# Performance work log

Hardware: AMD Instinct MI355X
Metric: run time of the kernel (lower is better)

The kernel has to match this reference:

```python
import jax, jax.numpy as jnp
import numpy as np

DIM = 192
HEADS = 6
WS = 8          # window_size
SHIFT = 4       # shift_size = window_size // 2
HID = DIM * 4   # mlp hidden
EPS = 1e-5


def _rel_index(ws):
    coords = np.stack(np.meshgrid(np.arange(ws), np.arange(ws), indexing='ij')).reshape(2, -1)
    rel = coords[:, :, None] - coords[:, None, :]
    rel = rel.transpose(1, 2, 0).copy()
    rel[:, :, 0] += ws - 1
    rel[:, :, 1] += ws - 1
    rel[:, :, 0] *= 2 * ws - 1
    return rel.sum(-1)  # [N, N] int


def _attn_mask(H, W, ws, ss):
    img = np.zeros((H, W), np.float32)
    sl = (slice(0, -ws), slice(-ws, -ss), slice(-ss, None))
    cnt = 0
    for h in sl:
        for w in sl:
            img[h, w] = cnt
            cnt += 1
    mw = img.reshape(H // ws, ws, W // ws, ws).transpose(0, 2, 1, 3).reshape(-1, ws * ws)
    am = mw[:, None, :] - mw[:, :, None]
    return np.where(am != 0, np.float32(-100.0), np.float32(0.0))  # [nW, N, N]


def _ln(x, w, b):
    m = x.mean(-1, keepdims=True)
    v = ((x - m) ** 2).mean(-1, keepdims=True)
    return (x - m) / jnp.sqrt(v + EPS) * w + b


def setup_inputs() -> dict:
    key = jax.random.key(0)
    ks = jax.random.split(key, 8)
    B, H, W = 8, 128, 128
    d = {
        'x': jax.random.normal(ks[0], (B, H * W, DIM), jnp.float32),
        'norm1_w': jnp.ones((DIM,), jnp.float32),
        'norm1_b': jnp.zeros((DIM,), jnp.float32),
        'qkv_w': jax.random.normal(ks[1], (DIM, 3 * DIM), jnp.float32) * 0.02,
        'qkv_b': jnp.zeros((3 * DIM,), jnp.float32),
        'rel_bias': jax.random.normal(ks[2], ((2 * WS - 1) ** 2, HEADS), jnp.float32) * 0.02,
        'proj_w': jax.random.normal(ks[3], (DIM, DIM), jnp.float32) * 0.02,
        'proj_b': jnp.zeros((DIM,), jnp.float32),
        'norm2_w': jnp.ones((DIM,), jnp.float32),
        'norm2_b': jnp.zeros((DIM,), jnp.float32),
        'mlp_w1': jax.random.normal(ks[4], (DIM, HID), jnp.float32) * 0.02,
        'mlp_b1': jnp.zeros((HID,), jnp.float32),
        'mlp_w2': jax.random.normal(ks[5], (HID, DIM), jnp.float32) * 0.02,
        'mlp_b2': jnp.zeros((DIM,), jnp.float32),
        'H': H,
        'W': W,
    }
    return d


def reference(x, norm1_w, norm1_b, qkv_w, qkv_b, rel_bias, proj_w, proj_b,
              norm2_w, norm2_b, mlp_w1, mlp_b1, mlp_w2, mlp_b2, H, W):
    B = x.shape[0]
    C, ws = DIM, WS
    N = ws * ws
    hd = C // HEADS
    shortcut = x
    h = _ln(x, norm1_w, norm1_b).reshape(B, H, W, C)
    if SHIFT > 0:
        h = jnp.roll(h, (-SHIFT, -SHIFT), axis=(1, 2))
    # window partition: (B,H,W,C) -> (B*nW, N, C)
    wins = h.reshape(B, H // ws, ws, W // ws, ws, C).transpose(0, 1, 3, 2, 4, 5).reshape(-1, N, C)
    qkv = (wins @ qkv_w + qkv_b).reshape(-1, N, 3, HEADS, hd).transpose(2, 0, 3, 1, 4)
    q, k, v = qkv[0] * (hd ** -0.5), qkv[1], qkv[2]
    attn = jnp.einsum('bhnd,bhmd->bhnm', q, k)
    ridx = jnp.asarray(_rel_index(ws))
    bias = rel_bias[ridx.reshape(-1)].reshape(N, N, HEADS).transpose(2, 0, 1)
    attn = attn + bias[None]
    if SHIFT > 0:
        am = jnp.asarray(_attn_mask(H, W, ws, SHIFT))  # [nW, N, N]
        nW = am.shape[0]
        attn = (attn.reshape(B, nW, HEADS, N, N) + am[None, :, None]).reshape(-1, HEADS, N, N)
    attn = jax.nn.softmax(attn, axis=-1)
    o = jnp.einsum('bhnm,bhmd->bhnd', attn, v).transpose(0, 2, 1, 3).reshape(-1, N, C)
    o = o @ proj_w + proj_b
    # window reverse: (B*nW, N, C) -> (B, H, W, C)
    o = o.reshape(B, H // ws, W // ws, ws, ws, C).transpose(0, 1, 3, 2, 4, 5).reshape(B, H, W, C)
    if SHIFT > 0:
        o = jnp.roll(o, (SHIFT, SHIFT), axis=(1, 2))
    x = shortcut + o.reshape(B, H * W, C)
    y = _ln(x, norm2_w, norm2_b)
    y = jax.nn.gelu(y @ mlp_w1 + mlp_b1, approximate=False) @ mlp_w2 + mlp_b2
    return x + y
```

## Files before the change

### kernel.cpp

```cpp
#include <hip/hip_runtime.h>
#include <hip/hip_bf16.h>
#include <math.h>

typedef __bf16 bf16;
typedef __bf16 bf16x8 __attribute__((ext_vector_type(8)));
typedef float f32x4 __attribute__((ext_vector_type(4)));

#define EPS 1e-5f

__device__ __forceinline__ int swz16(int row, int byteoff) {
  return byteoff ^ ((row & 7) << 4);
}

__device__ __forceinline__ void st_lds_bf16x2(char* lds, int off, float a, float b) {
  union { bf16 h[2]; unsigned u; } pk;
  pk.h[0] = (bf16)a; pk.h[1] = (bf16)b;
  *(unsigned*)(lds + off) = pk.u;
}

__device__ __forceinline__ void gl_lds16(const bf16* g, char* l) {
  __builtin_amdgcn_global_load_lds(
      (const __attribute__((address_space(1))) unsigned int*)(const void*)g,
      (__attribute__((address_space(3))) unsigned int*)l, 16, 0, 0);
}

__device__ __forceinline__ void bar_raw() {
  asm volatile("" ::: "memory");
  __builtin_amdgcn_s_barrier();
  asm volatile("" ::: "memory");
}

__global__ __launch_bounds__(256) void k_prep(
    const float* __restrict__ qkv_w, const float* __restrict__ proj_w,
    const float* __restrict__ mlp_w1, const float* __restrict__ mlp_w2,
    const float* __restrict__ rel_bias,
    bf16* __restrict__ w_qkv_t, bf16* __restrict__ w_proj_t,
    bf16* __restrict__ w_mlp1_t, bf16* __restrict__ w_mlp2_t,
    float* __restrict__ bias_tab) {
  int idx = blockIdx.x * 256 + threadIdx.x;
  if (idx < 110592) { int n = idx / 192, k = idx % 192; w_qkv_t[idx] = (bf16)qkv_w[k * 576 + n]; return; }
  idx -= 110592;
  if (idx < 36864) { int n = idx / 192, k = idx % 192; w_proj_t[idx] = (bf16)proj_w[k * 192 + n]; return; }
  idx -= 36864;
  if (idx < 147456) { int n = idx / 192, k = idx % 192; w_mlp1_t[idx] = (bf16)mlp_w1[k * 768 + n]; return; }
  idx -= 147456;
  if (idx < 147456) { int n = idx / 768, k = idx % 768; w_mlp2_t[idx] = (bf16)mlp_w2[k * 192 + n]; return; }
  idx -= 147456;
  {
    int h = idx >> 12, n = (idx >> 6) & 63, m = idx & 63;
    int i1 = n >> 3, j1 = n & 7, i2 = m >> 3, j2 = m & 7;
    int ridx = (i1 - i2 + 7) * 15 + (j1 - j2 + 7);
    bias_tab[idx] = rel_bias[ridx * 6 + h];
  }
}

__global__ __launch_bounds__(512) void k1a_ln(
    const float* __restrict__ x, const float* __restrict__ n1w, const float* __restrict__ n1b,
    bf16* __restrict__ xn) {
  const int win = blockIdx.x;
  const int bb = win >> 8, wi = (win >> 4) & 15, wj = win & 15;
  const int tid = threadIdx.x;
  const int t = tid >> 3, q = tid & 7;
  const int i = t >> 3, j = t & 7;
  const int oh = (wi * 8 + i + 4) & 127, ow = (wj * 8 + j + 4) & 127;
  const float* xr = x + (((size_t)bb * 128 + oh) * 128 + ow) * 192 + q * 24;
  float v[24];
  float s = 0.f, ss = 0.f;
#pragma unroll
  for (int u = 0; u < 6; ++u) {
    float4 f = ((const float4*)xr)[u];
    v[4 * u] = f.x; v[4 * u + 1] = f.y; v[4 * u + 2] = f.z; v[4 * u + 3] = f.w;
    s += (f.x + f.y) + (f.z + f.w);
    ss += (f.x * f.x + f.y * f.y) + (f.z * f.z + f.w * f.w);
  }
  s += __shfl_xor(s, 1); s += __shfl_xor(s, 2); s += __shfl_xor(s, 4);
  ss += __shfl_xor(ss, 1); ss += __shfl_xor(ss, 2); ss += __shfl_xor(ss, 4);
  const float mean = s * (1.f / 192.f);
  const float rstd = rsqrtf(ss * (1.f / 192.f) - mean * mean + EPS);
  union { bf16 h[24]; uint4 u4[3]; } pk;
#pragma unroll
  for (int u = 0; u < 24; ++u) {
    const int c = q * 24 + u;
    pk.h[u] = (bf16)((v[u] - mean) * rstd * n1w[c] + n1b[c]);
  }
  uint4* dst = (uint4*)(xn + ((size_t)win * 64 + t) * 192 + q * 24);
#pragma unroll
  for (int u = 0; u < 3; ++u) dst[u] = pk.u4[u];
}

__global__ __launch_bounds__(512, 4) void k1b_qkv(
    const bf16* __restrict__ xn, const bf16* __restrict__ wqkv, const float* __restrict__ qkvb,
    bf16* __restrict__ qbuf, bf16* __restrict__ kbuf, bf16* __restrict__ vtbuf) {
  __shared__ alignas(16) char ldsA[2][16384];
  __shared__ alignas(16) char ldsB[2][24576];
  const int blk = blockIdx.x, cb = blockIdx.y;
  const int tid = threadIdx.x;
  const int wid = tid >> 6, lane = tid & 63, lr = lane & 15, lg = lane >> 4;
  const int wr = wid >> 1, wc = wid & 1;
  const bf16* hA = xn + (size_t)blk * 128 * 192;
  const bf16* wB = wqkv + (size_t)cb * 192 * 192;

  auto stage = [&](int buf, int kt) {
    const int ko = kt * 64;
#pragma unroll
    for (int i = 0; i < 2; ++i) {
      const int slot = i * 512 + wid * 64 + lane;
      const int r = slot >> 3, c = slot & 7;
      gl_lds16(hA + (size_t)r * 192 + ko + ((c ^ (r & 7)) << 3),
               ldsA[buf] + (i * 512 + wid * 64) * 16);
    }
#pragma unroll
    for (int i = 0; i < 3; ++i) {
      const int slot = i * 512 + wid * 64 + lane;
      const int r = slot >> 3, c = slot & 7;
      gl_lds16(wB + (size_t)r * 192 + ko + ((c ^ (r & 7)) << 3),
               ldsB[buf] + (i * 512 + wid * 64) * 16);
    }
  };

  f32x4 acc[2][6] = {};
  stage(0, 0);
  int cur = 0;
  for (int kt = 0; kt < 3; ++kt) {
    if (kt < 2) {
      stage(cur ^ 1, kt + 1);
      asm volatile("s_waitcnt vmcnt(5)" ::: "memory");
    } else {
      asm volatile("s_waitcnt vmcnt(0)" ::: "memory");
    }
    bar_raw();
#pragma unroll
    for (int ks = 0; ks < 2; ++ks) {
      bf16x8 af[2];
#pragma unroll
      for (int rf = 0; rf < 2; ++rf) {
        const int row = wr * 32 + rf * 16 + lr;
        af[rf] = *(const bf16x8*)(ldsA[cur] + row * 128 + (((ks * 4 + lg) ^ (row & 7)) << 4));
      }
#pragma unroll
      for (int cf = 0; cf < 6; ++cf) {
        const int col = wc * 96 + cf * 16 + lr;
        const bf16x8 bfr = *(const bf16x8*)(ldsB[cur] + col * 128 + (((ks * 4 + lg) ^ (col & 7)) << 4));
#pragma unroll
        for (int rf = 0; rf < 2; ++rf)
          acc[rf][cf] = __builtin_amdgcn_mfma_f32_16x16x32_bf16(af[rf], bfr, acc[rf][cf], 0, 0, 0);
      }
    }
    bar_raw();
    cur ^= 1;
  }
  const float scale = 0.1767766952966369f;
  if (cb < 2) {
    bf16* dst = (cb == 0) ? qbuf : kbuf;
    const float sc = (cb == 0) ? scale : 1.f;
#pragma unroll
    for (int rf = 0; rf < 2; ++rf) {
#pragma unroll
      for (int jj = 0; jj < 4; ++jj) {
        const size_t grow = (size_t)blk * 128 + wr * 32 + rf * 16 + lg * 4 + jj;
#pragma unroll
        for (int cf = 0; cf < 6; ++cf) {
          const int col = wc * 96 + cf * 16 + lr;
          dst[grow * 192 + col] = (bf16)((acc[rf][cf][jj] + qkvb[cb * 192 + col]) * sc);
        }
      }
    }
  } else {
    char* vlds = (char*)ldsB;
#pragma unroll
    for (int cf = 0; cf < 6; ++cf) {
      const int col = wc * 96 + cf * 16 + lr;
      const float bias = qkvb[384 + col];
#pragma unroll
      for (int rf = 0; rf < 2; ++rf)
#pragma unroll
        for (int jj = 0; jj < 4; ++jj) {
          const int row = wr * 32 + rf * 16 + lg * 4 + jj;
          *(bf16*)(vlds + swz16(row, row * 384 + col * 2)) = (bf16)(acc[rf][cf][jj] + bias);
        }
    }
    __syncthreads();
#pragma unroll
    for (int it = 0; it < 12; ++it) {
      const int idx = it * 512 + tid;
      const int w = idx / 3072, rem = idx % 3072;
      const int d = rem >> 4, tg = rem & 15;
      union { ushort u[4]; uint2 v; } pk;
#pragma unroll
      for (int j = 0; j < 4; ++j) {
        const int row = w * 64 + tg * 4 + j;
        pk.u[j] = *(const ushort*)(vlds + swz16(row, row * 384 + d * 2));
      }
      const int head = d >> 5, dd = d & 31;
      const int win = blk * 2 + w;
      *(uint2*)(vtbuf + ((size_t)win * 6 + head) * 2048 + dd * 64 + tg * 4) = pk.v;
    }
  }
}

__global__ __launch_bounds__(384) void k2_attn(
    const bf16* __restrict__ qbuf, const bf16* __restrict__ kbuf,
    const bf16* __restrict__ vtbuf, const float* __restrict__ btab_all,
    bf16* __restrict__ obuf) {
  __shared__ alignas(16) char p_lds_all[6 * 64 * 128];
  const int win = blockIdx.x;
  const int head = threadIdx.x >> 6;
  char* p_lds = p_lds_all + head * 64 * 128;
  const int lane = threadIdx.x & 63, lr = lane & 15, lg = lane >> 4;
  const bf16* qb = qbuf + (size_t)win * 12288 + head * 32;
  const bf16* kb = kbuf + (size_t)win * 12288 + head * 32;
  const bf16* vb = vtbuf + ((size_t)win * 6 + head) * 2048;
  f32x4 sacc[4][4] = {};
  bf16x8 bk[4];
#pragma unroll
  for (int cf = 0; cf < 4; ++cf)
    bk[cf] = *(const bf16x8*)(kb + (size_t)(cf * 16 + lr) * 192 + lg * 8);
#pragma unroll
  for (int rf = 0; rf < 4; ++rf) {
    const bf16x8 aq = *(const bf16x8*)(qb + (size_t)(rf * 16 + lr) * 192 + lg * 8);
#pragma unroll
    for (int cf = 0; cf < 4; ++cf)
      sacc[rf][cf] = __builtin_amdgcn_mfma_f32_16x16x32_bf16(aq, bk[cf], sacc[rf][cf], 0, 0, 0);
  }
  const int wi = (win >> 4) & 15, wj = win & 15;
  const bool eh = (wi == 15), ew = (wj == 15);
  const float* btab = btab_all + head * 4096;
#pragma unroll
  for (int rf = 0; rf < 4; ++rf) {
#pragma unroll
    for (int jj = 0; jj < 4; ++jj) {
      const int n = rf * 16 + lg * 4 + jj;
      const int i1 = n >> 3, j1 = n & 7;
      float vals[4];
#pragma unroll
      for (int cf = 0; cf < 4; ++cf) {
        const int m = cf * 16 + lr;
        const int i2 = m >> 3, j2 = m & 7;
        float sv = sacc[rf][cf][jj] + btab[n * 64 + m];
        const bool msk = (eh && ((i1 >= 4) != (i2 >= 4))) || (ew && ((j1 >= 4) != (j2 >= 4)));
        if (msk) sv -= 100.f;
        vals[cf] = sv;
      }
      float mx = fmaxf(fmaxf(vals[0], vals[1]), fmaxf(vals[2], vals[3]));
      mx = fmaxf(mx, __shfl_xor(mx, 1));
      mx = fmaxf(mx, __shfl_xor(mx, 2));
      mx = fmaxf(mx, __shfl_xor(mx, 4));
      mx = fmaxf(mx, __shfl_xor(mx, 8));
      float sum = 0.f;
#pragma unroll
      for (int cf = 0; cf < 4; ++cf) { vals[cf] = __expf(vals[cf] - mx); sum += vals[cf]; }
      sum += __shfl_xor(sum, 1); sum += __shfl_xor(sum, 2);
      sum += __shfl_xor(sum, 4); sum += __shfl_xor(sum, 8);
      const float inv = 1.f / sum;
#pragma unroll
      for (int cf = 0; cf < 4; ++cf) {
        const int m = cf * 16 + lr;
        *(bf16*)(p_lds + swz16(n, n * 128 + m * 2)) = (bf16)(vals[cf] * inv);
      }
    }
  }
  __syncthreads();
  f32x4 oacc[4][2] = {};
#pragma unroll
  for (int ks = 0; ks < 2; ++ks) {
    bf16x8 pf[4];
#pragma unroll
    for (int rf = 0; rf < 4; ++rf) {
      const int row = rf * 16 + lr;
      pf[rf] = *(const bf16x8*)(p_lds + swz16(row, row * 128 + (ks * 32 + lg * 8) * 2));
    }
#pragma unroll
    for (int cf = 0; cf < 2; ++cf) {
      const bf16x8 vf = *(const bf16x8*)(vb + (cf * 16 + lr) * 64 + ks * 32 + lg * 8);
#pragma unroll
      for (int rf = 0; rf < 4; ++rf)
        oacc[rf][cf] = __builtin_amdgcn_mfma_f32_16x16x32_bf16(pf[rf], vf, oacc[rf][cf], 0, 0, 0);
    }
  }
  bf16* ob = obuf + (size_t)win * 64 * 192 + head * 32;
#pragma unroll
  for (int rf = 0; rf < 4; ++rf)
#pragma unroll
    for (int cf = 0; cf < 2; ++cf)
#pragma unroll
      for (int jj = 0; jj < 4; ++jj) {
        const int tok = rf * 16 + lg * 4 + jj;
        const int d = cf * 16 + lr;
        ob[(size_t)tok * 192 + d] = (bf16)oacc[rf][cf][jj];
      }
}

__global__ __launch_bounds__(512, 4) void k3_proj(
    const bf16* __restrict__ obuf, const bf16* __restrict__ wproj,
    const float* __restrict__ projb, const float* __restrict__ x,
    bf16* __restrict__ x2) {
  __shared__ alignas(16) char ldsA[2][16384];
  __shared__ alignas(16) char ldsB[2][24576];
  const int blk = blockIdx.x;
  const int tid = threadIdx.x;
  const int wid = tid >> 6, lane = tid & 63, lr = lane & 15, lg = lane >> 4;
  const int wr = wid >> 1, wc = wid & 1;
  const bf16* hA = obuf + (size_t)blk * 128 * 192;

  auto stage = [&](int buf, int kt) {
    const int ko = kt * 64;
#pragma unroll
    for (int i = 0; i < 2; ++i) {
      const int slot = i * 512 + wid * 64 + lane;
      const int r = slot >> 3, c = slot & 7;
      gl_lds16(hA + (size_t)r * 192 + ko + ((c ^ (r & 7)) << 3),
               ldsA[buf] + (i * 512 + wid * 64) * 16);
    }
#pragma unroll
    for (int i = 0; i < 3; ++i) {
      const int slot = i * 512 + wid * 64 + lane;
      const int r = slot >> 3, c = slot & 7;
      gl_lds16(wproj + (size_t)r * 192 + ko + ((c ^ (r & 7)) << 3),
               ldsB[buf] + (i * 512 + wid * 64) * 16);
    }
  };

  f32x4 acc[2][6] = {};
  stage(0, 0);
  int cur = 0;
  for (int kt = 0; kt < 3; ++kt) {
    if (kt < 2) {
      stage(cur ^ 1, kt + 1);
      asm volatile("s_waitcnt vmcnt(5)" ::: "memory");
    } else {
      asm volatile("s_waitcnt vmcnt(0)" ::: "memory");
    }
    bar_raw();
#pragma unroll
    for (int ks = 0; ks < 2; ++ks) {
      bf16x8 af[2];
#pragma unroll
      for (int rf = 0; rf < 2; ++rf) {
        const int row = wr * 32 + rf * 16 + lr;
        af[rf] = *(const bf16x8*)(ldsA[cur] + row * 128 + (((ks * 4 + lg) ^ (row & 7)) << 4));
      }
#pragma unroll
      for (int cf = 0; cf < 6; ++cf) {
        const int col = wc * 96 + cf * 16 + lr;
        const bf16x8 bfr = *(const bf16x8*)(ldsB[cur] + col * 128 + (((ks * 4 + lg) ^ (col & 7)) << 4));
#pragma unroll
        for (int rf = 0; rf < 2; ++rf)
          acc[rf][cf] = __builtin_amdgcn_mfma_f32_16x16x32_bf16(af[rf], bfr, acc[rf][cf], 0, 0, 0);
      }
    }
    bar_raw();
    cur ^= 1;
  }
#pragma unroll
  for (int rf = 0; rf < 2; ++rf) {
#pragma unroll
    for (int jj = 0; jj < 4; ++jj) {
      const int grow = blk * 128 + wr * 32 + rf * 16 + lg * 4 + jj;
      const int win = grow >> 6, t = grow & 63;
      const int bb = win >> 8, wi = (win >> 4) & 15, wj = win & 15;
      const int oh = (wi * 8 + (t >> 3) + 4) & 127, ow = (wj * 8 + (t & 7) + 4) & 127;
      const size_t orow = (((size_t)bb * 128 + oh) * 128 + ow) * 192;
#pragma unroll
      for (int cf = 0; cf < 6; ++cf) {
        const int col = wc * 96 + cf * 16 + lr;
        x2[orow + col] = (bf16)(x[orow + col] + acc[rf][cf][jj] + projb[col]);
      }
    }
  }
}

__global__ __launch_bounds__(512) void k4ln(
    const bf16* __restrict__ x2, const float* __restrict__ n2w, const float* __restrict__ n2b,
    bf16* __restrict__ xln) {
  const int tid = threadIdx.x;
  const int t = tid >> 3, q = tid & 7;
  const size_t row = (size_t)blockIdx.x * 64 + t;
  const bf16* xr = x2 + row * 192 + q * 24;
  float v[24];
  float s = 0.f, ss = 0.f;
#pragma unroll
  for (int u = 0; u < 3; ++u) {
    const bf16x8 f = ((const bf16x8*)xr)[u];
#pragma unroll
    for (int e = 0; e < 8; ++e) {
      const float fv = (float)f[e];
      v[8 * u + e] = fv;
      s += fv; ss += fv * fv;
    }
  }
  s += __shfl_xor(s, 1); s += __shfl_xor(s, 2); s += __shfl_xor(s, 4);
  ss += __shfl_xor(ss, 1); ss += __shfl_xor(ss, 2); ss += __shfl_xor(ss, 4);
  const float mean = s * (1.f / 192.f);
  const float rstd = rsqrtf(ss * (1.f / 192.f) - mean * mean + EPS);
  union { bf16 h[24]; uint4 u4[3]; } pk;
#pragma unroll
  for (int u = 0; u < 24; ++u) {
    const int c = q * 24 + u;
    pk.h[u] = (bf16)((v[u] - mean) * rstd * n2w[c] + n2b[c]);
  }
  uint4* dst = (uint4*)(xln + row * 192 + q * 24);
#pragma unroll
  for (int u = 0; u < 3; ++u) dst[u] = pk.u4[u];
}

__global__ __launch_bounds__(512, 4) void k4a_gemm(
    const bf16* __restrict__ xln, const bf16* __restrict__ w1t, const float* __restrict__ b1,
    bf16* __restrict__ h1) {
  __shared__ alignas(16) char ldsA[2][16384];
  __shared__ alignas(16) char ldsB[2][24576];
  const int blk = blockIdx.x, cb = blockIdx.y;
  const int tid = threadIdx.x;
  const int wid = tid >> 6, lane = tid & 63, lr = lane & 15, lg = lane >> 4;
  const int wr = wid >> 1, wc = wid & 1;
  const bf16* hA = xln + (size_t)blk * 128 * 192;
  const bf16* wB = w1t + (size_t)cb * 192 * 192;

  auto stage = [&](int buf, int kt) {
    const int ko = kt * 64;
#pragma unroll
    for (int i = 0; i < 2; ++i) {
      const int slot = i * 512 + wid * 64 + lane;
      const int r = slot >> 3, c = slot & 7;
      gl_lds16(hA + (size_t)r * 192 + ko + ((c ^ (r & 7)) << 3),
               ldsA[buf] + (i * 512 + wid * 64) * 16);
    }
#pragma unroll
    for (int i = 0; i < 3; ++i) {
      const int slot = i * 512 + wid * 64 + lane;
      const int r = slot >> 3, c = slot & 7;
      gl_lds16(wB + (size_t)r * 192 + ko + ((c ^ (r & 7)) << 3),
               ldsB[buf] + (i * 512 + wid * 64) * 16);
    }
  };

  f32x4 acc[2][6] = {};
  stage(0, 0);
  int cur = 0;
  for (int kt = 0; kt < 3; ++kt) {
    if (kt < 2) {
      stage(cur ^ 1, kt + 1);
      asm volatile("s_waitcnt vmcnt(5)" ::: "memory");
    } else {
      asm volatile("s_waitcnt vmcnt(0)" ::: "memory");
    }
    bar_raw();
#pragma unroll
    for (int ks = 0; ks < 2; ++ks) {
      bf16x8 af[2];
#pragma unroll
      for (int rf = 0; rf < 2; ++rf) {
        const int row = wr * 32 + rf * 16 + lr;
        af[rf] = *(const bf16x8*)(ldsA[cur] + row * 128 + (((ks * 4 + lg) ^ (row & 7)) << 4));
      }
#pragma unroll
      for (int cf = 0; cf < 6; ++cf) {
        const int col = wc * 96 + cf * 16 + lr;
        const bf16x8 bfr = *(const bf16x8*)(ldsB[cur] + col * 128 + (((ks * 4 + lg) ^ (col & 7)) << 4));
#pragma unroll
        for (int rf = 0; rf < 2; ++rf)
          acc[rf][cf] = __builtin_amdgcn_mfma_f32_16x16x32_bf16(af[rf], bfr, acc[rf][cf], 0, 0, 0);
      }
    }
    bar_raw();
    cur ^= 1;
  }
#pragma unroll
  for (int rf = 0; rf < 2; ++rf) {
#pragma unroll
    for (int jj = 0; jj < 4; ++jj) {
      const size_t grow = (size_t)blk * 128 + wr * 32 + rf * 16 + lg * 4 + jj;
#pragma unroll
      for (int cf = 0; cf < 6; ++cf) {
        const int col = wc * 96 + cf * 16 + lr;
        const float vv = acc[rf][cf][jj] + b1[cb * 192 + col];
        const float g = 0.5f * vv * (1.f + erff(vv * 0.70710678f));
        h1[grow * 768 + cb * 192 + col] = (bf16)g;
      }
    }
  }
}

__global__ __launch_bounds__(512, 4) void k4b_mlp2(
    const bf16* __restrict__ h1, const bf16* __restrict__ w2t,
    const float* __restrict__ b2, const bf16* __restrict__ x2,
    float* __restrict__ out) {
  __shared__ alignas(16) char ldsA[2][16384];
  __shared__ alignas(16) char ldsB[2][24576];
  const int blk = blockIdx.x;
  const int tid = threadIdx.x;
  const int wid = tid >> 6, lane = tid & 63, lr = lane & 15, lg = lane >> 4;
  const int wr = wid >> 1, wc = wid & 1;
  const bf16* hA = h1 + (size_t)blk * 128 * 768;

  auto stage = [&](int buf, int kt) {
    const int ko = kt * 64;
#pragma unroll
    for (int i = 0; i < 2; ++i) {
      const int slot = i * 512 + wid * 64 + lane;
      const int r = slot >> 3, c = slot & 7;
      gl_lds16(hA + (size_t)r * 768 + ko + ((c ^ (r & 7)) << 3),
               ldsA[buf] + (i * 512 + wid * 64) * 16);
    }
#pragma unroll
    for (int i = 0; i < 3; ++i) {
      const int slot = i * 512 + wid * 64 + lane;
      const int r = slot >> 3, c = slot & 7;
      gl_lds16(w2t + (size_t)r * 768 + ko + ((c ^ (r & 7)) << 3),
               ldsB[buf] + (i * 512 + wid * 64) * 16);
    }
  };

  f32x4 acc[2][6] = {};
  stage(0, 0);
  int cur = 0;
  for (int kt = 0; kt < 12; ++kt) {
    if (kt < 11) {
      stage(cur ^ 1, kt + 1);
      asm volatile("s_waitcnt vmcnt(5)" ::: "memory");
    } else {
      asm volatile("s_waitcnt vmcnt(0)" ::: "memory");
    }
    bar_raw();
#pragma unroll
    for (int ks = 0; ks < 2; ++ks) {
      bf16x8 af[2];
#pragma unroll
      for (int rf = 0; rf < 2; ++rf) {
        const int row = wr * 32 + rf * 16 + lr;
        af[rf] = *(const bf16x8*)(ldsA[cur] + row * 128 + (((ks * 4 + lg) ^ (row & 7)) << 4));
      }
#pragma unroll
      for (int cf = 0; cf < 6; ++cf) {
        const int col = wc * 96 + cf * 16 + lr;
        const bf16x8 bfr = *(const bf16x8*)(ldsB[cur] + col * 128 + (((ks * 4 + lg) ^ (col & 7)) << 4));
#pragma unroll
        for (int rf = 0; rf < 2; ++rf)
          acc[rf][cf] = __builtin_amdgcn_mfma_f32_16x16x32_bf16(af[rf], bfr, acc[rf][cf], 0, 0, 0);
      }
    }
    bar_raw();
    cur ^= 1;
  }
#pragma unroll
  for (int rf = 0; rf < 2; ++rf) {
#pragma unroll
    for (int jj = 0; jj < 4; ++jj) {
      const size_t grow = (size_t)blk * 128 + wr * 32 + rf * 16 + lg * 4 + jj;
#pragma unroll
      for (int cf = 0; cf < 6; ++cf) {
        const int col = wc * 96 + cf * 16 + lr;
        out[grow * 192 + col] = (float)x2[grow * 192 + col] + acc[rf][cf][jj] + b2[col];
      }
    }
  }
}

extern "C" void kernel_launch(void* const* d_in, const int* in_sizes, int n_in,
                              void* d_out, int out_size, void* d_ws, size_t ws_size,
                              hipStream_t stream) {
  (void)in_sizes; (void)n_in; (void)out_size; (void)ws_size;
  const float* x     = (const float*)d_in[0];
  const float* n1w   = (const float*)d_in[1];
  const float* n1b   = (const float*)d_in[2];
  const float* qkv_w = (const float*)d_in[3];
  const float* qkv_b = (const float*)d_in[4];
  const float* rel_b = (const float*)d_in[5];
  const float* proj_w= (const float*)d_in[6];
  const float* proj_b= (const float*)d_in[7];
  const float* n2w   = (const float*)d_in[8];
  const float* n2b   = (const float*)d_in[9];
  const float* w1    = (const float*)d_in[10];
  const float* b1    = (const float*)d_in[11];
  const float* w2    = (const float*)d_in[12];
  const float* b2    = (const float*)d_in[13];
  float* out = (float*)d_out;

  char* ws = (char*)d_ws;
  size_t off = 0;
  auto alloc = [&](size_t bytes) { char* p = ws + off; off += (bytes + 255) & ~(size_t)255; return p; };
  bf16* w_qkv_t  = (bf16*)alloc(576 * 192 * 2);
  bf16* w_proj_t = (bf16*)alloc(192 * 192 * 2);
  bf16* w_mlp1_t = (bf16*)alloc(768 * 192 * 2);
  bf16* w_mlp2_t = (bf16*)alloc(192 * 768 * 2);
  float* bias_tab = (float*)alloc(6 * 64 * 64 * 4);
  bf16* xn    = (bf16*)alloc((size_t)131072 * 192 * 2);
  bf16* qbuf  = (bf16*)alloc((size_t)131072 * 192 * 2);
  bf16* kbuf  = (bf16*)alloc((size_t)131072 * 192 * 2);
  bf16* vtbuf = (bf16*)alloc((size_t)2048 * 6 * 64 * 32 * 2);
  bf16* obuf  = (bf16*)alloc((size_t)131072 * 192 * 2);
  bf16* x2    = (bf16*)alloc((size_t)131072 * 192 * 2);
  bf16* h1  = xn;
  bf16* xln = obuf;

  k_prep<<<1824, 256, 0, stream>>>(qkv_w, proj_w, w1, w2, rel_b,
                                   w_qkv_t, w_proj_t, w_mlp1_t, w_mlp2_t, bias_tab);
  k1a_ln<<<2048, 512, 0, stream>>>(x, n1w, n1b, xn);
  k1b_qkv<<<dim3(1024, 3), 512, 0, stream>>>(xn, w_qkv_t, qkv_b, qbuf, kbuf, vtbuf);
  k2_attn<<<2048, 384, 0, stream>>>(qbuf, kbuf, vtbuf, bias_tab, obuf);
  k3_proj<<<1024, 512, 0, stream>>>(obuf, w_proj_t, proj_b, x, x2);
  k4ln<<<2048, 512, 0, stream>>>(x2, n2w, n2b, xln);
  k4a_gemm<<<dim3(1024, 4), 512, 0, stream>>>(xln, w_mlp1_t, b1, h1);
  k4b_mlp2<<<1024, 512, 0, stream>>>(h1, w_mlp2_t, b2, x2, out);
}
```

Before: 452.0 us.

## Restructure MLP2 GEMM: A fragments from global, triple-buffered weights, 4 waves

The second MLP GEMM now runs with 256 threads. Each wave owns 32 full rows across all 192 output columns. Activation fragments are loaded straight from global memory into registers instead of being staged through LDS. Only the weight tile is staged in LDS, now triple-buffered, which drops the trailing barrier per k-step. This cuts LDS traffic and barriers but doubles the accumulator registers per wave, lowers occupancy, and exposes uncoalesced global loads of A directly to the MFMA loop.

```diff
diff --git a/kernel.cpp b/kernel.cpp
--- a/kernel.cpp
+++ b/kernel.cpp
@@ -480,75 +480,71 @@
   }
 }
 
-__global__ __launch_bounds__(512, 4) void k4b_mlp2(
+__global__ __launch_bounds__(256, 2) void k4b_mlp2(
     const bf16* __restrict__ h1, const bf16* __restrict__ w2t,
     const float* __restrict__ b2, const bf16* __restrict__ x2,
     float* __restrict__ out) {
-  __shared__ alignas(16) char ldsA[2][16384];
-  __shared__ alignas(16) char ldsB[2][24576];
+  __shared__ alignas(16) char ldsB[3][24576];
   const int blk = blockIdx.x;
   const int tid = threadIdx.x;
   const int wid = tid >> 6, lane = tid & 63, lr = lane & 15, lg = lane >> 4;
-  const int wr = wid >> 1, wc = wid & 1;
-  const bf16* hA = h1 + (size_t)blk * 128 * 768;
-
-  auto stage = [&](int buf, int kt) {
+  const bf16* hA = h1 + ((size_t)blk * 128 + wid * 32) * 768;
+
+  auto stageB = [&](int buf, int kt) {
     const int ko = kt * 64;
 #pragma unroll
-    for (int i = 0; i < 2; ++i) {
-      const int slot = i * 512 + wid * 64 + lane;
-      const int r = slot >> 3, c = slot & 7;
-      gl_lds16(hA + (size_t)r * 768 + ko + ((c ^ (r & 7)) << 3),
-               ldsA[buf] + (i * 512 + wid * 64) * 16);
-    }
-#pragma unroll
-    for (int i = 0; i < 3; ++i) {
-      const int slot = i * 512 + wid * 64 + lane;
+    for (int i = 0; i < 6; ++i) {
+      const int slot = i * 256 + wid * 64 + lane;
       const int r = slot >> 3, c = slot & 7;
       gl_lds16(w2t + (size_t)r * 768 + ko + ((c ^ (r & 7)) << 3),
-               ldsB[buf] + (i * 512 + wid * 64) * 16);
+               ldsB[buf] + (i * 256 + wid * 64) * 16);
     }
   };
 
-  f32x4 acc[2][6] = {};
-  stage(0, 0);
-  int cur = 0;
+  f32x4 acc[2][12] = {};
+  stageB(0, 0);
+  int cur = 0, nxt = 1;
   for (int kt = 0; kt < 12; ++kt) {
+    bf16x8 a0[2], a1[2];
+#pragma unroll
+    for (int rf = 0; rf < 2; ++rf) {
+      const bf16* ar = hA + (size_t)(rf * 16 + lr) * 768 + kt * 64 + lg * 8;
+      a0[rf] = *(const bf16x8*)(ar);
+      a1[rf] = *(const bf16x8*)(ar + 32);
+    }
     if (kt < 11) {
-      stage(cur ^ 1, kt + 1);
-      asm volatile("s_waitcnt vmcnt(5)" ::: "memory");
+      stageB(nxt, kt + 1);
+      asm volatile("s_waitcnt vmcnt(10)" ::: "memory");
     } else {
-      asm volatile("s_waitcnt vmcnt(0)" ::: "memory");
+      asm volatile("s_waitcnt vmcnt(4)" ::: "memory");
     }
     bar_raw();
+    const char* bcur = ldsB[cur];
 #pragma unroll
     for (int ks = 0; ks < 2; ++ks) {
-      bf16x8 af[2];
-#pragma unroll
-      for (int rf = 0; rf < 2; ++rf) {
-        const int row = wr * 32 + rf * 16 + lr;
-        af[rf] = *(const bf16x8*)(ldsA[cur] + row * 128 + (((ks * 4 + lg) ^ (row & 7)) << 4));
-      }
-#pragma unroll
-      for (int cf = 0; cf < 6; ++cf) {
-        const int col = wc * 96 + cf * 16 + lr;
-        const bf16x8 bfr = *(const bf16x8*)(ldsB[cur] + col * 128 + (((ks * 4 + lg) ^ (col & 7)) << 4));
-#pragma unroll
-        for (int rf = 0; rf < 2; ++rf)
-          acc[rf][cf] = __builtin_amdgcn_mfma_f32_16x16x32_bf16(af[rf], bfr, acc[rf][cf], 0, 0, 0);
-      }
-    }
-    bar_raw();
-    cur ^= 1;
+#pragma unroll
+      for (int cf = 0; cf < 12; ++cf) {
+        const int col = cf * 16 + lr;
+        const bf16x8 bfr = *(const bf16x8*)(bcur + col * 128 + (((ks * 4 + lg) ^ (col & 7)) << 4));
+        if (ks == 0) {
+          acc[0][cf] = __builtin_amdgcn_mfma_f32_16x16x32_bf16(a0[0], bfr, acc[0][cf], 0, 0, 0);
+          acc[1][cf] = __builtin_amdgcn_mfma_f32_16x16x32_bf16(a0[1], bfr, acc[1][cf], 0, 0, 0);
+        } else {
+          acc[0][cf] = __builtin_amdgcn_mfma_f32_16x16x32_bf16(a1[0], bfr, acc[0][cf], 0, 0, 0);
+          acc[1][cf] = __builtin_amdgcn_mfma_f32_16x16x32_bf16(a1[1], bfr, acc[1][cf], 0, 0, 0);
+        }
+      }
+    }
+    cur = nxt; nxt = (nxt == 2) ? 0 : nxt + 1;
   }
 #pragma unroll
   for (int rf = 0; rf < 2; ++rf) {
 #pragma unroll
     for (int jj = 0; jj < 4; ++jj) {
-      const size_t grow = (size_t)blk * 128 + wr * 32 + rf * 16 + lg * 4 + jj;
-#pragma unroll
-      for (int cf = 0; cf < 6; ++cf) {
-        const int col = wc * 96 + cf * 16 + lr;
+      const size_t grow = (size_t)blk * 128 + wid * 32 + rf * 16 + lg * 4 + jj;
+#pragma unroll
+      for (int cf = 0; cf < 12; ++cf) {
+        const int col = cf * 16 + lr;
         out[grow * 192 + col] = (float)x2[grow * 192 + col] + acc[rf][cf][jj] + b2[col];
       }
     }
@@ -600,5 +596,5 @@
   k3_proj<<<1024, 512, 0, stream>>>(obuf, w_proj_t, proj_b, x, x2);
   k4ln<<<2048, 512, 0, stream>>>(x2, n2w, n2b, xln);
   k4a_gemm<<<dim3(1024, 4), 512, 0, stream>>>(xln, w_mlp1_t, b1, h1);
-  k4b_mlp2<<<1024, 512, 0, stream>>>(h1, w_mlp2_t, b2, x2, out);
-}
+  k4b_mlp2<<<1024, 256, 0, stream>>>(h1, w_mlp2_t, b2, x2, out);
+}
```

Result: faster. 429.3 us (-5.0%).
